# Kernel tuning notes

Hardware: AMD Instinct MI355X
Metric: run time of the kernel (lower is better)

## Reference

```python
import jax, jax.numpy as jnp
import numpy as np

N = 10000
E = 640000
IN_CH = 512
OUT_CH = 256
K = 2


def setup_inputs() -> dict:
    key = jax.random.key(0)
    k1, k2, k3, k4, k5 = jax.random.split(key, 5)
    x = jax.random.normal(k1, (N, IN_CH), dtype=jnp.float32)
    edge_index = jax.random.randint(k2, (2, E), 0, N, dtype=jnp.int64)
    lin_w = jax.random.normal(k3, (OUT_CH, IN_CH), dtype=jnp.float32) * (1.0 / np.sqrt(IN_CH))
    lin_b = jax.random.normal(k4, (OUT_CH,), dtype=jnp.float32) * 0.01
    weights = jax.random.uniform(k5, (K,), dtype=jnp.float32)
    return {"x": x, "edge_index": edge_index, "lin_w": lin_w, "lin_b": lin_b, "weights": weights}


def reference(x, edge_index, lin_w, lin_b, weights):
    n = x.shape[0]
    row, col = edge_index[0], edge_index[1]
    # deg = bincount(row); symmetric-normalized edge weights
    deg = jax.ops.segment_sum(jnp.ones(row.shape[0], dtype=x.dtype), row, num_segments=n)
    deg_inv_sqrt = jnp.where(deg > 0, jax.lax.rsqrt(deg), 0.0)
    norm = deg_inv_sqrt[row] * deg_inv_sqrt[col]  # [E]

    def spmm(h):
        # y[i] = sum_{e: row[e]==i} norm[e] * h[col[e]]
        return jax.ops.segment_sum(norm[:, None] * h[col], row, num_segments=n)

    out = x @ lin_w.T + lin_b  # [N, OUT_CH]
    # Faithful ARMA loop: x_k starts from the CURRENT accumulated `out` each hop-group
    for k in range(K):
        x_k = out
        for _ in range(k + 1):
            x_k = spmm(x_k)
        out = out + weights[k] * x_k
    return out
```

## Files before the change

kernel.cpp:

```cpp
#include <hip/hip_runtime.h>

#define N_NODES 10000
#define E_EDGES 640000
#define IN_CH   512
#define OUT_CH  256
#define HALF_CH 128
#define CSR_CAP (E_EDGES + 16 * N_NODES + 128)
#define G_GEMM_X 157
#define G_GEMM  (G_GEMM_X * 2)
#define HBLK    125
#define EPB     5120
#define G_CONVX 2500
#define G_CONVW 64
#define G_AB    40

typedef short bf16x8 __attribute__((ext_vector_type(8)));
typedef float f32x4  __attribute__((ext_vector_type(4)));

__device__ __forceinline__ unsigned short f2b(float f) {
    unsigned int u = __float_as_uint(f);
    return (unsigned short)((u + 0x7FFFu + ((u >> 16) & 1u)) >> 16);
}
__device__ __forceinline__ float lo16(unsigned int u) { return __uint_as_float(u << 16); }
__device__ __forceinline__ float hi16(unsigned int u) { return __uint_as_float(u & 0xFFFF0000u); }
__device__ __forceinline__ float b2f(unsigned short u) { return __uint_as_float(((unsigned int)u) << 16); }

__global__ __launch_bounds__(256) void conv_hist(const float* __restrict__ x,
                                                 const float* __restrict__ w,
                                                 unsigned short* __restrict__ xb,
                                                 unsigned short* __restrict__ wb,
                                                 const int* __restrict__ row,
                                                 int* __restrict__ cnt,
                                                 unsigned short* __restrict__ rank) {
    int bid = blockIdx.x;
    int tid = threadIdx.x;
    if (bid < HBLK) {
        __shared__ int hist[N_NODES];
        for (int i = tid; i < N_NODES; i += 256) hist[i] = 0;
        __syncthreads();
        int ebase = bid * EPB;
        for (int i = tid; i < EPB; i += 256) {
            int r = row[ebase + i];
            rank[ebase + i] = (unsigned short)atomicAdd(&hist[r], 1);
        }
        __syncthreads();
        int* cb = cnt + (size_t)bid * N_NODES;
        for (int i = tid; i < N_NODES; i += 256) cb[i] = hist[i];
        return;
    }
    int u = bid - HBLK;
    const float* src;
    unsigned short* dst;
    size_t base;
    if (u < G_CONVX) { src = x;  dst = xb; base = (size_t)u * 2048 + tid * 8; }
    else             { src = w;  dst = wb; base = (size_t)(u - G_CONVX) * 2048 + tid * 8; }
    float4 a = *(const float4*)(src + base);
    float4 b = *(const float4*)(src + base + 4);
    ushort4 lo, hi;
    lo.x = f2b(a.x); lo.y = f2b(a.y); lo.z = f2b(a.z); lo.w = f2b(a.w);
    hi.x = f2b(b.x); hi.y = f2b(b.y); hi.z = f2b(b.z); hi.w = f2b(b.w);
    *(ushort4*)(dst + base) = lo;
    *(ushort4*)(dst + base + 4) = hi;
}

__global__ __launch_bounds__(256) void alloc_a2(int* __restrict__ cnt,
                                                int2* __restrict__ pd,
                                                float* __restrict__ dinv, float* __restrict__ sq,
                                                int* __restrict__ pads, int n) {
    int r = blockIdx.x * 256 + threadIdx.x;
    if (r >= n) return;
    int run = 0;
    int b0 = 0;
    for (; b0 + 8 <= HBLK; b0 += 8) {
        int c[8];
        #pragma unroll
        for (int j = 0; j < 8; j++) c[j] = cnt[(size_t)(b0 + j) * N_NODES + r];
        #pragma unroll
        for (int j = 0; j < 8; j++) {
            cnt[(size_t)(b0 + j) * N_NODES + r] = run;
            run += c[j];
        }
    }
    for (; b0 < HBLK; b0++) {
        int c = cnt[(size_t)b0 * N_NODES + r];
        cnt[(size_t)b0 * N_NODES + r] = run;
        run += c;
    }
    int d = run;
    int pad = (d + 15) & ~15;
    dinv[r] = (d > 0) ? rsqrtf((float)d) : 0.0f;
    sq[r]   = (d > 0) ? sqrtf((float)d) : 0.0f;
    pd[r] = make_int2(d, pad);
    pads[r] = pad;
}

__global__ __launch_bounds__(1024) void scan_pads(const int* __restrict__ pads,
                                                  int* __restrict__ rowstart, int n) {
    __shared__ int ls[1024];
    int t = threadIdx.x;
    int base = t * 10;
    int loc[10];
    int sum = 0;
    if (base < n) {
        #pragma unroll
        for (int i = 0; i < 10; i++) { loc[i] = pads[base + i]; sum += loc[i]; }
    }
    ls[t] = sum;
    __syncthreads();
    for (int off = 1; off < 1024; off <<= 1) {
        int v = (t >= off) ? ls[t - off] : 0;
        __syncthreads();
        ls[t] += v;
        __syncthreads();
    }
    if (base < n) {
        int run = ls[t] - sum;
        #pragma unroll
        for (int i = 0; i < 10; i++) { rowstart[base + i] = run; run += loc[i]; }
    }
}

__global__ __launch_bounds__(256) void gemm_scatter_ab(const unsigned short* __restrict__ xb,
                                                       const unsigned short* __restrict__ wb,
                                                       const float* __restrict__ bias,
                                                       const float* __restrict__ dinv,
                                                       unsigned short* __restrict__ h0b,
                                                       const int* __restrict__ row,
                                                       const int* __restrict__ col,
                                                       const int* __restrict__ base,
                                                       const int* __restrict__ rowstart,
                                                       const unsigned short* __restrict__ rank,
                                                       unsigned short* __restrict__ csr_col,
                                                       const int2* __restrict__ pd,
                                                       int2* __restrict__ seg) {
    __shared__ __align__(16) char smem[40960];
    int bid = blockIdx.x;
    int tid = threadIdx.x;
    if (bid >= G_GEMM + HBLK) {
        int r = (bid - G_GEMM - HBLK) * 256 + tid;
        if (r >= N_NODES) return;
        int s = rowstart[r];
        int2 pd_ = pd[r];
        seg[r] = make_int2(s, s + pd_.y);
        for (int j = pd_.x; j < pd_.y; j++) csr_col[s + j] = (unsigned short)N_NODES;
        return;
    }
    if (bid >= G_GEMM) {
        int sb = bid - G_GEMM;
        int* bs = (int*)smem;
        const int4* cb4 = (const int4*)(base + (size_t)sb * N_NODES);
        const int4* rs4 = (const int4*)rowstart;
        for (int i = tid; i < N_NODES / 4; i += 256) {
            int4 c = cb4[i];
            int4 r = rs4[i];
            int4 o;
            o.x = c.x + r.x; o.y = c.y + r.y; o.z = c.z + r.z; o.w = c.w + r.w;
            ((int4*)bs)[i] = o;
        }
        __syncthreads();
        int ebase = sb * EPB;
        for (int i = tid; i < EPB; i += 256) {
            int e = ebase + i;
            int p = bs[row[e]] + (int)rank[e];
            csr_col[p] = (unsigned short)col[e];
        }
        return;
    }
    typedef unsigned short us72[72];
    us72* As = (us72*)smem;
    us72* Bs = (us72*)(smem + 64 * 72 * 2);
    int bx = bid % G_GEMM_X;
    int plane = bid / G_GEMM_X;
    int wave = tid >> 6, lane = tid & 63, quad = lane >> 4, l16 = lane & 15;
    int row0 = bx * 64;
    int n0 = plane * 128;
    unsigned short* h0b_p = h0b + (size_t)plane * (N_NODES + 1) * HALF_CH;

    int ar = tid >> 2;
    int aseg = (tid & 3) * 16;
    int br = tid >> 1;
    int bseg = (tid & 1) * 32;

    f32x4 acc[8] = {};
    for (int k0 = 0; k0 < IN_CH; k0 += 64) {
        {
            int gr = row0 + ar;
            if (gr < N_NODES) {
                const uint4* src = (const uint4*)(xb + (size_t)gr * IN_CH + k0 + aseg);
                *(uint4*)&As[ar][aseg]     = src[0];
                *(uint4*)&As[ar][aseg + 8] = src[1];
            } else {
                uint4 z = {0, 0, 0, 0};
                *(uint4*)&As[ar][aseg]     = z;
                *(uint4*)&As[ar][aseg + 8] = z;
            }
        }
        {
            const uint4* src = (const uint4*)(wb + (size_t)(n0 + br) * IN_CH + k0 + bseg);
            *(uint4*)&Bs[br][bseg]      = src[0];
            *(uint4*)&Bs[br][bseg + 8]  = src[1];
            *(uint4*)&Bs[br][bseg + 16] = src[2];
            *(uint4*)&Bs[br][bseg + 24] = src[3];
        }
        __syncthreads();
        #pragma unroll
        for (int kk = 0; kk < 2; kk++) {
            bf16x8 a = *(const bf16x8*)&As[wave * 16 + l16][kk * 32 + quad * 8];
            #pragma unroll
            for (int t = 0; t < 8; t++) {
                bf16x8 b = *(const bf16x8*)&Bs[t * 16 + l16][kk * 32 + quad * 8];
                acc[t] = __builtin_amdgcn_mfma_f32_16x16x32_bf16(a, b, acc[t], 0, 0, 0);
            }
        }
        __syncthreads();
    }
    #pragma unroll
    for (int t = 0; t < 8; t++) {
        int lcol = t * 16 + l16;
        float bv = bias[n0 + lcol];
        #pragma unroll
        for (int r = 0; r < 4; r++) {
            int grow = row0 + wave * 16 + quad * 4 + r;
            if (grow < N_NODES) {
                float v = acc[t][r] + bv;
                h0b_p[(size_t)grow * HALF_CH + lcol] = f2b(v * dinv[grow]);
            }
        }
    }
    if (bx == 0 && tid < 64)
        ((unsigned int*)(h0b_p + (size_t)N_NODES * HALF_CH))[tid] = 0u;
}

__global__ __launch_bounds__(256) void spmm_kernel(const unsigned short* __restrict__ hb,
                                                   const int2* __restrict__ seg,
                                                   const unsigned short* __restrict__ csr_col,
                                                   const float* __restrict__ dinv,
                                                   const float* __restrict__ sq,
                                                   const unsigned short* __restrict__ prev_b,
                                                   const float* __restrict__ wts, int widx,
                                                   unsigned short* __restrict__ yb_out,
                                                   float* __restrict__ axpy_out,
                                                   unsigned short* __restrict__ axpyb_out,
                                                   int n) {
    int plane = blockIdx.x & 1;
    int node = (blockIdx.x >> 1) * 4 + (threadIdx.x >> 6);
    int lane = threadIdx.x & 63;
    if (node >= n) return;
    int sub = lane >> 4, l16 = lane & 15;
    size_t pstride = (size_t)(n + 1) * HALF_CH;
    const unsigned short* hp = hb + (size_t)plane * pstride;

    int2 se = seg[node];
    int s = se.x, e = se.y;
    float acc[8] = {0.f, 0.f, 0.f, 0.f, 0.f, 0.f, 0.f, 0.f};
    if (s < e) {
        int cA0 = csr_col[s + 0  + sub];
        int cA1 = csr_col[s + 4  + sub];
        int cA2 = csr_col[s + 8  + sub];
        int cA3 = csr_col[s + 12 + sub];
        uint4 vA0 = *(const uint4*)(hp + (size_t)cA0 * HALF_CH + l16 * 8);
        uint4 vA1 = *(const uint4*)(hp + (size_t)cA1 * HALF_CH + l16 * 8);
        uint4 vA2 = *(const uint4*)(hp + (size_t)cA2 * HALF_CH + l16 * 8);
        uint4 vA3 = *(const uint4*)(hp + (size_t)cA3 * HALF_CH + l16 * 8);
        int cB0 = csr_col[s + 16 + sub];
        int cB1 = csr_col[s + 20 + sub];
        int cB2 = csr_col[s + 24 + sub];
        int cB3 = csr_col[s + 28 + sub];
        int p = s;
        while (p + 16 < e) {
            uint4 vB0 = *(const uint4*)(hp + (size_t)cB0 * HALF_CH + l16 * 8);
            uint4 vB1 = *(const uint4*)(hp + (size_t)cB1 * HALF_CH + l16 * 8);
            uint4 vB2 = *(const uint4*)(hp + (size_t)cB2 * HALF_CH + l16 * 8);
            uint4 vB3 = *(const uint4*)(hp + (size_t)cB3 * HALF_CH + l16 * 8);
            int pn = p + 32;
            int cC0 = csr_col[pn + 0  + sub];
            int cC1 = csr_col[pn + 4  + sub];
            int cC2 = csr_col[pn + 8  + sub];
            int cC3 = csr_col[pn + 12 + sub];
            acc[0] += lo16(vA0.x) + lo16(vA1.x) + lo16(vA2.x) + lo16(vA3.x);
            acc[1] += hi16(vA0.x) + hi16(vA1.x) + hi16(vA2.x) + hi16(vA3.x);
            acc[2] += lo16(vA0.y) + lo16(vA1.y) + lo16(vA2.y) + lo16(vA3.y);
            acc[3] += hi16(vA0.y) + hi16(vA1.y) + hi16(vA2.y) + hi16(vA3.y);
            acc[4] += lo16(vA0.z) + lo16(vA1.z) + lo16(vA2.z) + lo16(vA3.z);
            acc[5] += hi16(vA0.z) + hi16(vA1.z) + hi16(vA2.z) + hi16(vA3.z);
            acc[6] += lo16(vA0.w) + lo16(vA1.w) + lo16(vA2.w) + lo16(vA3.w);
            acc[7] += hi16(vA0.w) + hi16(vA1.w) + hi16(vA2.w) + hi16(vA3.w);
            vA0 = vB0; vA1 = vB1; vA2 = vB2; vA3 = vB3;
            cB0 = cC0; cB1 = cC1; cB2 = cC2; cB3 = cC3;
            p += 16;
        }
        acc[0] += lo16(vA0.x) + lo16(vA1.x) + lo16(vA2.x) + lo16(vA3.x);
        acc[1] += hi16(vA0.x) + hi16(vA1.x) + hi16(vA2.x) + hi16(vA3.x);
        acc[2] += lo16(vA0.y) + lo16(vA1.y) + lo16(vA2.y) + lo16(vA3.y);
        acc[3] += hi16(vA0.y) + hi16(vA1.y) + hi16(vA2.y) + hi16(vA3.y);
        acc[4] += lo16(vA0.z) + lo16(vA1.z) + lo16(vA2.z) + lo16(vA3.z);
        acc[5] += hi16(vA0.z) + hi16(vA1.z) + hi16(vA2.z) + hi16(vA3.z);
        acc[6] += lo16(vA0.w) + lo16(vA1.w) + lo16(vA2.w) + lo16(vA3.w);
        acc[7] += hi16(vA0.w) + hi16(vA1.w) + hi16(vA2.w) + hi16(vA3.w);
    }
    #pragma unroll
    for (int k = 0; k < 8; k++) {
        acc[k] += __shfl_xor(acc[k], 16, 64);
        acc[k] += __shfl_xor(acc[k], 32, 64);
    }
    if (sub != 0) return;

    float di = dinv[node];
    float y[8];
    #pragma unroll
    for (int k = 0; k < 8; k++) y[k] = di * acc[k];

    size_t pbase = (size_t)plane * pstride + (size_t)node * HALF_CH + l16 * 8;
    size_t padrow = (size_t)plane * pstride + (size_t)n * HALF_CH + l16 * 8;
    if (yb_out) {
        ushort4 o0, o1;
        o0.x = f2b(di * y[0]); o0.y = f2b(di * y[1]); o0.z = f2b(di * y[2]); o0.w = f2b(di * y[3]);
        o1.x = f2b(di * y[4]); o1.y = f2b(di * y[5]); o1.z = f2b(di * y[6]); o1.w = f2b(di * y[7]);
        *(ushort4*)(yb_out + pbase) = o0;
        *(ushort4*)(yb_out + pbase + 4) = o1;
        if (node == 0) {
            ushort4 z = {0, 0, 0, 0};
            *(ushort4*)(yb_out + padrow) = z;
            *(ushort4*)(yb_out + padrow + 4) = z;
        }
    }
    if (prev_b) {
        float wk = wts[widx];
        float sqn = sq[node];
        ushort4 p0 = *(const ushort4*)(prev_b + pbase);
        ushort4 p1 = *(const ushort4*)(prev_b + pbase + 4);
        float o[8];
        o[0] = b2f(p0.x) * sqn + wk * y[0];
        o[1] = b2f(p0.y) * sqn + wk * y[1];
        o[2] = b2f(p0.z) * sqn + wk * y[2];
        o[3] = b2f(p0.w) * sqn + wk * y[3];
        o[4] = b2f(p1.x) * sqn + wk * y[4];
        o[5] = b2f(p1.y) * sqn + wk * y[5];
        o[6] = b2f(p1.z) * sqn + wk * y[6];
        o[7] = b2f(p1.w) * sqn + wk * y[7];
        if (axpy_out) {
            size_t fbase = (size_t)node * OUT_CH + plane * HALF_CH + l16 * 8;
            float4 f0 = {o[0], o[1], o[2], o[3]};
            float4 f1 = {o[4], o[5], o[6], o[7]};
            *(float4*)(axpy_out + fbase) = f0;
            *(float4*)(axpy_out + fbase + 4) = f1;
        }
        if (axpyb_out) {
            ushort4 b0, b1;
            b0.x = f2b(di * o[0]); b0.y = f2b(di * o[1]); b0.z = f2b(di * o[2]); b0.w = f2b(di * o[3]);
            b1.x = f2b(di * o[4]); b1.y = f2b(di * o[5]); b1.z = f2b(di * o[6]); b1.w = f2b(di * o[7]);
            *(ushort4*)(axpyb_out + pbase) = b0;
            *(ushort4*)(axpyb_out + pbase + 4) = b1;
            if (node == 0) {
                ushort4 z = {0, 0, 0, 0};
                *(ushort4*)(axpyb_out + padrow) = z;
                *(ushort4*)(axpyb_out + padrow + 4) = z;
            }
        }
    }
}

extern "C" void kernel_launch(void* const* d_in, const int* in_sizes, int n_in,
                              void* d_out, int out_size, void* d_ws, size_t ws_size,
                              hipStream_t stream) {
    const float* x     = (const float*)d_in[0];
    const int*   ei    = (const int*)d_in[1];
    const float* lin_w = (const float*)d_in[2];
    const float* lin_b = (const float*)d_in[3];
    const float* wts   = (const float*)d_in[4];
    float* out = (float*)d_out;

    char* ws = (char*)d_ws;
    size_t off = 0;
    auto alloc = [&](size_t bytes) -> void* {
        void* p = ws + off;
        off += (bytes + 255) & ~(size_t)255;
        return p;
    };
    int*   cnt      = (int*)  alloc((size_t)HBLK * N_NODES * 4);
    unsigned short* rank = (unsigned short*)alloc((size_t)E_EDGES * 2);
    int2*  pd       = (int2*) alloc((size_t)N_NODES * 8);
    int*   pads     = (int*)  alloc((size_t)N_NODES * 4);
    int*   rowstart = (int*)  alloc((size_t)N_NODES * 4);
    int2*  seg      = (int2*) alloc((size_t)N_NODES * 8);
    float* dinv     = (float*)alloc(N_NODES * 4);
    float* sq       = (float*)alloc(N_NODES * 4);
    unsigned short* csr_col = (unsigned short*)alloc((size_t)CSR_CAP * 2);
    unsigned short* xb = (unsigned short*)alloc((size_t)N_NODES * IN_CH * 2);
    unsigned short* wb = (unsigned short*)alloc((size_t)OUT_CH * IN_CH * 2);
    unsigned short* h0b   = (unsigned short*)alloc((size_t)2 * (N_NODES + 1) * HALF_CH * 2);
    unsigned short* out1b = (unsigned short*)alloc((size_t)2 * (N_NODES + 1) * HALF_CH * 2);
    unsigned short* t2b   = (unsigned short*)alloc((size_t)2 * (N_NODES + 1) * HALF_CH * 2);

    const int* row = ei;
    const int* col = ei + E_EDGES;

    conv_hist<<<HBLK + G_CONVX + G_CONVW, 256, 0, stream>>>(x, lin_w, xb, wb,
                                                            row, cnt, rank);
    alloc_a2<<<(N_NODES + 255) / 256, 256, 0, stream>>>(cnt, pd, dinv, sq, pads, N_NODES);
    scan_pads<<<1, 1024, 0, stream>>>(pads, rowstart, N_NODES);
    gemm_scatter_ab<<<G_GEMM + HBLK + G_AB, 256, 0, stream>>>(xb, wb, lin_b, dinv, h0b,
                                                              row, col, cnt, rowstart,
                                                              rank, csr_col, pd, seg);

    int sgrid = 2 * ((N_NODES + 3) / 4);
    spmm_kernel<<<sgrid, 256, 0, stream>>>(h0b, seg, csr_col, dinv, sq, h0b,
                                           wts, 0, nullptr, nullptr, out1b, N_NODES);
    spmm_kernel<<<sgrid, 256, 0, stream>>>(out1b, seg, csr_col, dinv, sq, nullptr,
                                           wts, 0, t2b, nullptr, nullptr, N_NODES);
    spmm_kernel<<<sgrid, 256, 0, stream>>>(t2b, seg, csr_col, dinv, sq, out1b,
                                           wts, 1, nullptr, out, nullptr, N_NODES);
}
```

Before: 179.3 us.

## Fuse three SpMM launches into one cooperative kernel with grid syncs

```diff
diff --git a/kernel.cpp b/kernel.cpp
--- a/kernel.cpp
+++ b/kernel.cpp
@@ -1,4 +1,7 @@
 #include <hip/hip_runtime.h>
+#include <hip/hip_cooperative_groups.h>
+
+namespace cg = cooperative_groups;
 
 #define N_NODES 10000
 #define E_EDGES 640000
@@ -13,6 +16,7 @@
 #define G_CONVX 2500
 #define G_CONVW 64
 #define G_AB    40
+#define UNITS   (2 * ((N_NODES + 3) / 4))
 
 typedef short bf16x8 __attribute__((ext_vector_type(8)));
 typedef float f32x4  __attribute__((ext_vector_type(4)));
@@ -231,19 +235,19 @@
         ((unsigned int*)(h0b_p + (size_t)N_NODES * HALF_CH))[tid] = 0u;
 }
 
-__global__ __launch_bounds__(256) void spmm_kernel(const unsigned short* __restrict__ hb,
-                                                   const int2* __restrict__ seg,
-                                                   const unsigned short* __restrict__ csr_col,
-                                                   const float* __restrict__ dinv,
-                                                   const float* __restrict__ sq,
-                                                   const unsigned short* __restrict__ prev_b,
-                                                   const float* __restrict__ wts, int widx,
-                                                   unsigned short* __restrict__ yb_out,
-                                                   float* __restrict__ axpy_out,
-                                                   unsigned short* __restrict__ axpyb_out,
-                                                   int n) {
-    int plane = blockIdx.x & 1;
-    int node = (blockIdx.x >> 1) * 4 + (threadIdx.x >> 6);
+__device__ __forceinline__ void spmm_unit(int u, int n,
+                                          const unsigned short* __restrict__ hb,
+                                          const int2* __restrict__ seg,
+                                          const unsigned short* __restrict__ csr_col,
+                                          const float* __restrict__ dinv,
+                                          const float* __restrict__ sq,
+                                          const unsigned short* __restrict__ prev_b,
+                                          const float* __restrict__ wts, int widx,
+                                          unsigned short* __restrict__ yb_out,
+                                          float* __restrict__ axpy_out,
+                                          unsigned short* __restrict__ axpyb_out) {
+    int plane = u & 1;
+    int node = (u >> 1) * 4 + (threadIdx.x >> 6);
     int lane = threadIdx.x & 63;
     if (node >= n) return;
     int sub = lane >> 4, l16 = lane & 15;
@@ -360,6 +364,30 @@
     }
 }
 
+__global__ __launch_bounds__(256) void spmm3_coop(const unsigned short* __restrict__ h0b,
+                                                  unsigned short* __restrict__ out1b,
+                                                  unsigned short* __restrict__ t2b,
+                                                  const int2* __restrict__ seg,
+                                                  const unsigned short* __restrict__ csr_col,
+                                                  const float* __restrict__ dinv,
+                                                  const float* __restrict__ sq,
+                                                  const float* __restrict__ wts,
+                                                  float* __restrict__ out, int n) {
+    cg::grid_group grid = cg::this_grid();
+    int gdim = gridDim.x;
+    for (int u = blockIdx.x; u < UNITS; u += gdim)
+        spmm_unit(u, n, h0b, seg, csr_col, dinv, sq, h0b, wts, 0,
+                  nullptr, nullptr, out1b);
+    grid.sync();
+    for (int u = blockIdx.x; u < UNITS; u += gdim)
+        spmm_unit(u, n, out1b, seg, csr_col, dinv, sq, nullptr, wts, 0,
+                  t2b, nullptr, nullptr);
+    grid.sync();
+    for (int u = blockIdx.x; u < UNITS; u += gdim)
+        spmm_unit(u, n, t2b, seg, csr_col, dinv, sq, out1b, wts, 1,
+                  nullptr, out, nullptr);
+}
+
 extern "C" void kernel_launch(void* const* d_in, const int* in_sizes, int n_in,
                               void* d_out, int out_size, void* d_ws, size_t ws_size,
                               hipStream_t stream) {
@@ -403,11 +431,24 @@
                                                               row, col, cnt, rowstart,
                                                               rank, csr_col, pd, seg);
 
-    int sgrid = 2 * ((N_NODES + 3) / 4);
-    spmm_kernel<<<sgrid, 256, 0, stream>>>(h0b, seg, csr_col, dinv, sq, h0b,
-                                           wts, 0, nullptr, nullptr, out1b, N_NODES);
-    spmm_kernel<<<sgrid, 256, 0, stream>>>(out1b, seg, csr_col, dinv, sq, nullptr,
-                                           wts, 0, t2b, nullptr, nullptr, N_NODES);
-    spmm_kernel<<<sgrid, 256, 0, stream>>>(t2b, seg, csr_col, dinv, sq, out1b,
-                                           wts, 1, nullptr, out, nullptr, N_NODES);
-}
+    static int coopGrid = 0;
+    if (coopGrid == 0) {
+        int dev = 0;
+        hipGetDevice(&dev);
+        int numCU = 0;
+        hipDeviceGetAttribute(&numCU, hipDeviceAttributeMultiprocessorCount, dev);
+        int occ = 0;
+        hipOccupancyMaxActiveBlocksPerMultiprocessor(&occ, spmm3_coop, 256, 0);
+        long g = (long)occ * (long)numCU;
+        if (g > UNITS) g = UNITS;
+        if (g < 256) g = 256;
+        coopGrid = (int)g;
+    }
+    int nn = N_NODES;
+    void* kargs[] = {
+        (void*)&h0b, (void*)&out1b, (void*)&t2b, (void*)&seg, (void*)&csr_col,
+        (void*)&dinv, (void*)&sq, (void*)&wts, (void*)&out, (void*)&nn
+    };
+    hipLaunchCooperativeKernel((void*)spmm3_coop, dim3(coopGrid), dim3(256),
+                               kargs, 0, stream);
+}
```

Measured after the change: 476.6 us. +165.8%, slower.
